# Performance work log

Hardware: AMD Instinct MI355X
Metric: run time of the kernel (lower is better)

The kernel has to match this reference:

```python
import jax, jax.numpy as jnp
import numpy as np

UNITS = 1000


def gru_step(x, h, W, U, b):
    # Keras GRU, reset_after=True. b: [2, 3*units] = (input bias, recurrent bias)
    gx = x @ W + b[0]
    gh = h @ U + b[1]
    xz, xr, xh = jnp.split(gx, 3, axis=-1)
    hz, hr, hh_ = jnp.split(gh, 3, axis=-1)
    z = jax.nn.sigmoid(xz + hz)
    r = jax.nn.sigmoid(xr + hr)
    hh = jnp.tanh(xh + r * hh_)
    return z * h + (1.0 - z) * hh


def setup_inputs() -> dict:
    key = jax.random.key(0)
    ks = jax.random.split(key, 12)
    V1, E, U = 32001, 100, UNITS
    B, S = 64, 25
    sc = 0.05
    return {
        "x": jax.random.randint(ks[0], (B, S), 0, V1, dtype=jnp.int32),
        "target": jax.random.randint(ks[1], (B, S), 0, V1, dtype=jnp.int32),
        "start_token": 2,
        "emb_table": jax.random.normal(ks[2], (V1, E), jnp.float32) * sc,
        "enc_kernel": jax.random.normal(ks[3], (E, 3 * U), jnp.float32) * sc,
        "enc_recurrent": jax.random.normal(ks[4], (U, 3 * U), jnp.float32) * sc,
        "enc_bias": jax.random.normal(ks[5], (2, 3 * U), jnp.float32) * sc,
        "dec_kernel": jax.random.normal(ks[6], (E, 3 * U), jnp.float32) * sc,
        "dec_recurrent": jax.random.normal(ks[7], (U, 3 * U), jnp.float32) * sc,
        "dec_bias": jax.random.normal(ks[8], (2, 3 * U), jnp.float32) * sc,
        "fc_w": jax.random.normal(ks[9], (U, V1), jnp.float32) * sc,
        "fc_b": jnp.zeros((V1,), jnp.float32),
    }


def reference(x, target, start_token, emb_table, enc_kernel, enc_recurrent,
              enc_bias, dec_kernel, dec_recurrent, dec_bias, fc_w, fc_b):
    B, S = x.shape
    max_len = target.shape[1]

    # ---- Encoder (computed faithfully; its output is unused downstream,
    # matching the original where attention is never invoked) ----
    emb_x = emb_table[x]                      # [B,S,E]
    mask_x = (x != 0)                          # mask_zero embedding

    def enc_scan(h, xm):
        xt, mt = xm                            # xt:[B,E], mt:[B]
        hn = gru_step(xt, h, enc_kernel, enc_recurrent, enc_bias)
        h = jnp.where(mt[:, None], hn, h)      # masked steps carry state
        return h, h

    h0 = jnp.zeros((B, UNITS), emb_x.dtype)
    enc_state, enc_out = jax.lax.scan(
        enc_scan, h0, (jnp.swapaxes(emb_x, 0, 1), jnp.swapaxes(mask_x, 0, 1)))

    # ---- Decoder: original calls gru WITHOUT initial_state, so every step
    # starts from a zero hidden state -> all timesteps are independent. ----
    # teacher-forced inputs: [start_token, target[:, :-1]]
    tokens = jnp.concatenate(
        [jnp.full((B, 1), start_token, dtype=target.dtype), target[:, :-1]], axis=1)  # [B,T]
    emb_d = emb_table[tokens]                  # [B,T,E]
    mask_d = (tokens != 0)                     # [B,T]

    h_zero = jnp.zeros((B, max_len, UNITS), emb_d.dtype)
    h1 = gru_step(emb_d, h_zero, dec_kernel, dec_recurrent, dec_bias)  # [B,T,U]
    # masked single step -> output is the zero initial output
    h1 = jnp.where(mask_d[..., None], h1, 0.0)

    logits = h1 @ fc_w + fc_b                  # [B,T,V+1]
    app_emb = logits.astype(jnp.float32) @ emb_table  # [B,T,E]
    return app_emb
```

## Files before the change

### kernel.cpp

```cpp
#include <hip/hip_runtime.h>

typedef _Float16 half_t;
typedef _Float16 half8 __attribute__((ext_vector_type(8)));
typedef float    floatx4 __attribute__((ext_vector_type(4)));

#define V1     32001
#define EMBD   100
#define UNITS  1000
#define SEQ    25
#define NROWS  1600
#define KPAD   32032
#define HSTR   1024
#define NKB    32
#define PROWS  1024

__global__ __launch_bounds__(256) void kPre(
    const float* __restrict__ E, half_t* __restrict__ ET,
    const float* __restrict__ fcb, float* __restrict__ vvec,
    const int* __restrict__ target, const int* __restrict__ stok,
    const float* __restrict__ K, const float* __restrict__ bias,
    half_t* __restrict__ h1h)
{
    __shared__ char smem[100 * 66 * sizeof(half_t)];
    const int tid = threadIdx.x;
    const int bid = blockIdx.x;

    if (bid < 501) {
        half_t* lds = (half_t*)smem;
        const int k0 = bid * 64;
        const int e  = tid & 127;
        const int kh = tid >> 7;
        for (int kk = kh; kk < 64; kk += 2) {
            const int k = k0 + kk;
            float v = 0.f;
            if (k < 32000 && e < 100) v = E[k * 100 + e];
            if (e < 100) lds[e * 66 + kk] = (half_t)v;
        }
        __syncthreads();
        const int kl = tid & 63;
        const int eh = tid >> 6;
        if (k0 + kl < KPAD) {
            for (int ee = eh; ee < 100; ee += 4)
                ET[(long)ee * KPAD + k0 + kl] = lds[ee * 66 + kl];
        }
        return;
    }

    if (bid < 757) {
        const int e  = tid & 127;
        const int g  = tid >> 7;
        const int ec = min(e, 99);
        const int slice = (bid - 501) * 2 + g;
        const int chunk = (V1 + 511) / 512;
        const int j0 = slice * chunk;
        const int j1 = min(j0 + chunk, V1);
        float acc = 0.f;
        for (int j = j0; j < j1; ++j)
            acc += fcb[j] * E[j * 100 + ec];
        if (e < 100) atomicAdd(&vvec[e], acc);
        return;
    }

    float (*xs)[100] = (float(*)[100])smem;
    __shared__ int msk[8];
    const int b3    = bid - 757;
    const int rg    = b3 % 200;
    const int uc    = b3 / 200;
    const int ibase = rg * 8;
    {
        const int r = tid >> 5, c = tid & 31;
        const int i = ibase + r;
        const int bb = i / SEQ, t = i - bb * SEQ;
        const int token = (t == 0) ? stok[0] : target[bb * SEQ + t - 1];
        if (c == 0) msk[r] = (token != 0);
        for (int cc = c; cc < 100; cc += 32)
            xs[r][cc] = E[token * 100 + cc];
    }
    __syncthreads();

    const int u = uc * 256 + tid;
    if (u < UNITS) {
        float az[8], ar[8], ah[8];
#pragma unroll
        for (int r = 0; r < 8; ++r) { az[r] = 0.f; ar[r] = 0.f; ah[r] = 0.f; }
#pragma unroll 4
        for (int k = 0; k < 100; ++k) {
            const float wz = K[k * 3000 + u];
            const float wr = K[k * 3000 + 1000 + u];
            const float wh = K[k * 3000 + 2000 + u];
#pragma unroll
            for (int r = 0; r < 8; ++r) {
                const float x = xs[r][k];
                az[r] += x * wz;
                ar[r] += x * wr;
                ah[r] += x * wh;
            }
        }
        const float* b0 = bias;
        const float* b1 = bias + 3000;
        const float bz  = b0[u] + b1[u];
        const float br  = b0[1000 + u] + b1[1000 + u];
        const float bh0 = b0[2000 + u];
        const float bh1 = b1[2000 + u];
#pragma unroll
        for (int r = 0; r < 8; ++r) {
            const float z   = 1.f / (1.f + __expf(-(az[r] + bz)));
            const float rg_ = 1.f / (1.f + __expf(-(ar[r] + br)));
            const float pre = ah[r] + bh0 + rg_ * bh1;
            const float ex  = __expf(2.f * pre);
            const float hh  = 1.f - 2.f / (ex + 1.f);
            h1h[(ibase + r) * HSTR + u] = (half_t)(msk[r] ? (1.f - z) * hh : 0.f);
        }
    } else {
        const half_t cv = (half_t)((u == 1000) ? 1.f : 0.f);
#pragma unroll
        for (int r = 0; r < 8; ++r)
            h1h[(ibase + r) * HSTR + u] = cv;
    }
}

__global__ __launch_bounds__(256) void kA(const float* __restrict__ W,
                                          const half_t* __restrict__ ET,
                                          float* __restrict__ P)
{
    __shared__ float red[3][64][57];
    const int tid   = threadIdx.x;
    const int lane  = tid & 63;
    const int wv    = tid >> 6;
    const int mb    = blockIdx.x;
    const int kb    = blockIdx.y;
    const int row16 = lane & 15;
    const int quad  = lane >> 4;

    const int m0  = mb * 32 + row16;
    const int mc0 = min(m0, UNITS - 1);
    const int mc1 = min(m0 + 16, UNITS - 1);

    const int ub = kb * 32;
    const int ue = min(ub + 32, 1000);
    const int pw = (ue - ub + 3) >> 2;
    const int wb = ub + wv * pw;
    const int we = min(wb + pw, ue);

    floatx4 acc0[7], acc1[7];
#pragma unroll
    for (int t = 0; t < 7; ++t) {
        acc0[t] = (floatx4){0.f, 0.f, 0.f, 0.f};
        acc1[t] = (floatx4){0.f, 0.f, 0.f, 0.f};
    }

    const float* wrow0 = W + (long)mc0 * V1;
    const float* wrow1 = W + (long)mc1 * V1;
    const half_t* bbase[7];
#pragma unroll
    for (int t = 0; t < 7; ++t) {
        const int nc = min(t * 16 + row16, 99);
        bbase[t] = ET + (long)nc * KPAD + quad * 8;
    }

    int un = wb;
    for (; un + 2 <= we; un += 2) {
        float f[2][16];
#pragma unroll
        for (int j = 0; j < 2; ++j) {
            const int k0 = (un + j) * 32 + quad * 8;
            __builtin_memcpy(&f[j][0], wrow0 + k0, 32);
            __builtin_memcpy(&f[j][8], wrow1 + k0, 32);
        }
#pragma unroll
        for (int j = 0; j < 2; ++j) {
            half8 a0, a1;
#pragma unroll
            for (int q = 0; q < 8; ++q) {
                a0[q] = (half_t)f[j][q];
                a1[q] = (half_t)f[j][8 + q];
            }
            const int koff = (un + j) * 32;
#pragma unroll
            for (int t = 0; t < 7; ++t) {
                const half8 b = *(const half8*)(bbase[t] + koff);
                acc0[t] = __builtin_amdgcn_mfma_f32_16x16x32_f16(a0, b, acc0[t], 0, 0, 0);
                acc1[t] = __builtin_amdgcn_mfma_f32_16x16x32_f16(a1, b, acc1[t], 0, 0, 0);
            }
        }
    }
    for (; un < we; ++un) {
        const int k0 = un * 32 + quad * 8;
        float f0[8], f1[8];
        __builtin_memcpy(f0, wrow0 + k0, 32);
        __builtin_memcpy(f1, wrow1 + k0, 32);
        half8 a0, a1;
#pragma unroll
        for (int q = 0; q < 8; ++q) { a0[q] = (half_t)f0[q]; a1[q] = (half_t)f1[q]; }
#pragma unroll
        for (int t = 0; t < 7; ++t) {
            const half8 b = *(const half8*)(bbase[t] + un * 32);
            acc0[t] = __builtin_amdgcn_mfma_f32_16x16x32_f16(a0, b, acc0[t], 0, 0, 0);
            acc1[t] = __builtin_amdgcn_mfma_f32_16x16x32_f16(a1, b, acc1[t], 0, 0, 0);
        }
    }

    if (wv > 0) {
#pragma unroll
        for (int t = 0; t < 7; ++t)
#pragma unroll
            for (int r = 0; r < 4; ++r) {
                red[wv - 1][lane][t * 4 + r]      = acc0[t][r];
                red[wv - 1][lane][28 + t * 4 + r] = acc1[t][r];
            }
    }
    __syncthreads();
    if (wv == 0) {
        float* Pk = P + (long)kb * (PROWS * 100);
        const int orow0 = mb * 32 + quad * 4;
#pragma unroll
        for (int t = 0; t < 7; ++t) {
            const int col = t * 16 + row16;
            if (col < 100) {
#pragma unroll
                for (int r = 0; r < 4; ++r) {
                    const int i = t * 4 + r;
                    const float s0 = acc0[t][r] + red[0][lane][i]
                                   + red[1][lane][i] + red[2][lane][i];
                    const float s1 = acc1[t][r] + red[0][lane][28 + i]
                                   + red[1][lane][28 + i] + red[2][lane][28 + i];
                    Pk[(orow0 + r) * 100 + col]      = s0;
                    Pk[(orow0 + 16 + r) * 100 + col] = s1;
                }
            }
        }
    }
}

__global__ __launch_bounds__(256) void kPost(const float* __restrict__ P,
                                             const float* __restrict__ W,
                                             const float* __restrict__ E,
                                             const float* __restrict__ vvec,
                                             half_t* __restrict__ MbT)
{
    const int idx = blockIdx.x * 256 + threadIdx.x;
    const int kk  = idx / 100;
    const int e   = idx - kk * 100;
    float s;
    if (kk < 1000) {
        s = 0.f;
#pragma unroll
        for (int kb = 0; kb < NKB; ++kb)
            s += P[(long)kb * (PROWS * 100) + kk * 100 + e];
        s += W[(long)kk * V1 + 32000] * E[32000 * 100 + e];
    } else if (kk == 1000) {
        s = vvec[e];
    } else {
        s = 0.f;
    }
    MbT[e * HSTR + kk] = (half_t)s;
}

__global__ __launch_bounds__(256) void kC(const half_t* __restrict__ h1h,
                                          const half_t* __restrict__ MbT,
                                          float* __restrict__ out)
{
    __shared__ float red[3][64][29];
    const int tid   = threadIdx.x;
    const int lane  = tid & 63;
    const int wv    = tid >> 6;
    const int rb    = blockIdx.x;
    const int row16 = lane & 15;
    const int quad  = lane >> 4;

    const half_t* arow = h1h + (long)(rb * 16 + row16) * HSTR + quad * 8;
    const half_t* bbase[7];
#pragma unroll
    for (int t = 0; t < 7; ++t) {
        const int nc = min(t * 16 + row16, 99);
        bbase[t] = MbT + (long)nc * HSTR + quad * 8;
    }

    floatx4 acc[7];
#pragma unroll
    for (int t = 0; t < 7; ++t) acc[t] = (floatx4){0.f, 0.f, 0.f, 0.f};

    const int wb = wv * 8;
#pragma unroll 2
    for (int un = wb; un < wb + 8; ++un) {
        const half8 a = *(const half8*)(arow + un * 32);
#pragma unroll
        for (int t = 0; t < 7; ++t) {
            const half8 b = *(const half8*)(bbase[t] + un * 32);
            acc[t] = __builtin_amdgcn_mfma_f32_16x16x32_f16(a, b, acc[t], 0, 0, 0);
        }
    }

    if (wv > 0) {
#pragma unroll
        for (int t = 0; t < 7; ++t)
#pragma unroll
            for (int r = 0; r < 4; ++r)
                red[wv - 1][lane][t * 4 + r] = acc[t][r];
    }
    __syncthreads();
    if (wv == 0) {
        const int orow0 = rb * 16 + quad * 4;
#pragma unroll
        for (int t = 0; t < 7; ++t) {
            const int col = t * 16 + row16;
            if (col < 100) {
#pragma unroll
                for (int r = 0; r < 4; ++r) {
                    const int i = t * 4 + r;
                    out[(orow0 + r) * 100 + col] = acc[t][r] + red[0][lane][i]
                        + red[1][lane][i] + red[2][lane][i];
                }
            }
        }
    }
}

extern "C" void kernel_launch(void* const* d_in, const int* in_sizes, int n_in,
                              void* d_out, int out_size, void* d_ws, size_t ws_size,
                              hipStream_t stream)
{
    const int*   target     = (const int*)d_in[1];
    const int*   start_tok  = (const int*)d_in[2];
    const float* emb        = (const float*)d_in[3];
    const float* dec_kernel = (const float*)d_in[7];
    const float* dec_bias   = (const float*)d_in[9];
    const float* fc_w       = (const float*)d_in[10];
    const float* fc_b       = (const float*)d_in[11];

    float*  vvec = (float*)d_ws;
    half_t* ET   = (half_t*)(vvec + 128);
    half_t* h1h  = ET + (size_t)100 * KPAD;
    half_t* MbT  = h1h + (size_t)NROWS * HSTR;
    float*  P    = (float*)(MbT + (size_t)100 * HSTR);
    float*  out  = (float*)d_out;

    hipMemsetAsync(vvec, 0, 128 * sizeof(float), stream);

    kPre<<<1557, 256, 0, stream>>>(emb, ET, fc_b, vvec, target, start_tok,
                                   dec_kernel, dec_bias, h1h);
    kA<<<dim3(32, NKB), 256, 0, stream>>>(fc_w, ET, P);
    kPost<<<(PROWS * 100) / 256, 256, 0, stream>>>(P, fc_w, emb, vvec, MbT);
    kC<<<100, 256, 0, stream>>>(h1h, MbT, out);
}
```

Before: 318.6 us.

## Give each kA wave its own row tile and drop the in-block LDS reduction

kA is restructured so that each wave owns a separate 16-row slice of fc_w (64 rows per block) instead of the four waves splitting K and reducing through LDS. The K split moves entirely to the grid: 36 chunks of 28 units, with the partials summed later in kPost. The inner loop now batches loads for four K-steps before issuing the MFMAs, to keep more memory requests in flight. In exchange, each B (embedding) fragment now feeds one MFMA instead of two, so embedding reads roughly double, and there are more partial slices for kPost to read and sum.

```diff
diff --git a/kernel.cpp b/kernel.cpp
--- a/kernel.cpp
+++ b/kernel.cpp
@@ -11,7 +11,8 @@
 #define NROWS  1600
 #define KPAD   32032
 #define HSTR   1024
-#define NKB    32
+#define NKB    36
+#define KUQ    28
 #define PROWS  1024
 
 __global__ __launch_bounds__(256) void kPre(
@@ -123,111 +124,81 @@
                                           const half_t* __restrict__ ET,
                                           float* __restrict__ P)
 {
-    __shared__ float red[3][64][57];
     const int tid   = threadIdx.x;
     const int lane  = tid & 63;
     const int wv    = tid >> 6;
-    const int mb    = blockIdx.x;
-    const int kb    = blockIdx.y;
+    const int mgrp  = blockIdx.x;
+    const int kq    = blockIdx.y;
     const int row16 = lane & 15;
     const int quad  = lane >> 4;
 
-    const int m0  = mb * 32 + row16;
-    const int mc0 = min(m0, UNITS - 1);
-    const int mc1 = min(m0 + 16, UNITS - 1);
-
-    const int ub = kb * 32;
-    const int ue = min(ub + 32, 1000);
-    const int pw = (ue - ub + 3) >> 2;
-    const int wb = ub + wv * pw;
-    const int we = min(wb + pw, ue);
-
-    floatx4 acc0[7], acc1[7];
-#pragma unroll
-    for (int t = 0; t < 7; ++t) {
-        acc0[t] = (floatx4){0.f, 0.f, 0.f, 0.f};
-        acc1[t] = (floatx4){0.f, 0.f, 0.f, 0.f};
-    }
-
-    const float* wrow0 = W + (long)mc0 * V1;
-    const float* wrow1 = W + (long)mc1 * V1;
-    const half_t* bbase[7];
+    const int m  = mgrp * 64 + wv * 16 + row16;
+    const int mc = min(m, UNITS - 1);
+    const float* wrow = W + (long)mc * V1;
+
+    const int wb = kq * KUQ;
+    const int we = min(wb + KUQ, 1000);
+
+    floatx4 acc[7];
+#pragma unroll
+    for (int t = 0; t < 7; ++t) acc[t] = (floatx4){0.f, 0.f, 0.f, 0.f};
+
+    const half_t* bb[7];
 #pragma unroll
     for (int t = 0; t < 7; ++t) {
         const int nc = min(t * 16 + row16, 99);
-        bbase[t] = ET + (long)nc * KPAD + quad * 8;
+        bb[t] = ET + (long)nc * KPAD + quad * 8;
     }
 
     int un = wb;
-    for (; un + 2 <= we; un += 2) {
-        float f[2][16];
-#pragma unroll
-        for (int j = 0; j < 2; ++j) {
+    for (; un + 4 <= we; un += 4) {
+        float fa[4][8];
+        half8 vb[4][7];
+#pragma unroll
+        for (int j = 0; j < 4; ++j) {
             const int k0 = (un + j) * 32 + quad * 8;
-            __builtin_memcpy(&f[j][0], wrow0 + k0, 32);
-            __builtin_memcpy(&f[j][8], wrow1 + k0, 32);
-        }
-#pragma unroll
-        for (int j = 0; j < 2; ++j) {
-            half8 a0, a1;
-#pragma unroll
-            for (int q = 0; q < 8; ++q) {
-                a0[q] = (half_t)f[j][q];
-                a1[q] = (half_t)f[j][8 + q];
-            }
+            __builtin_memcpy(&fa[j][0], wrow + k0, 32);
+        }
+#pragma unroll
+        for (int j = 0; j < 4; ++j) {
             const int koff = (un + j) * 32;
 #pragma unroll
-            for (int t = 0; t < 7; ++t) {
-                const half8 b = *(const half8*)(bbase[t] + koff);
-                acc0[t] = __builtin_amdgcn_mfma_f32_16x16x32_f16(a0, b, acc0[t], 0, 0, 0);
-                acc1[t] = __builtin_amdgcn_mfma_f32_16x16x32_f16(a1, b, acc1[t], 0, 0, 0);
-            }
+            for (int t = 0; t < 7; ++t)
+                vb[j][t] = *(const half8*)(bb[t] + koff);
+        }
+#pragma unroll
+        for (int j = 0; j < 4; ++j) {
+            half8 a;
+#pragma unroll
+            for (int q = 0; q < 8; ++q) a[q] = (half_t)fa[j][q];
+#pragma unroll
+            for (int t = 0; t < 7; ++t)
+                acc[t] = __builtin_amdgcn_mfma_f32_16x16x32_f16(a, vb[j][t], acc[t], 0, 0, 0);
         }
     }
     for (; un < we; ++un) {
         const int k0 = un * 32 + quad * 8;
-        float f0[8], f1[8];
-        __builtin_memcpy(f0, wrow0 + k0, 32);
-        __builtin_memcpy(f1, wrow1 + k0, 32);
-        half8 a0, a1;
-#pragma unroll
-        for (int q = 0; q < 8; ++q) { a0[q] = (half_t)f0[q]; a1[q] = (half_t)f1[q]; }
+        float f0[8];
+        __builtin_memcpy(f0, wrow + k0, 32);
+        half8 a;
+#pragma unroll
+        for (int q = 0; q < 8; ++q) a[q] = (half_t)f0[q];
 #pragma unroll
         for (int t = 0; t < 7; ++t) {
-            const half8 b = *(const half8*)(bbase[t] + un * 32);
-            acc0[t] = __builtin_amdgcn_mfma_f32_16x16x32_f16(a0, b, acc0[t], 0, 0, 0);
-            acc1[t] = __builtin_amdgcn_mfma_f32_16x16x32_f16(a1, b, acc1[t], 0, 0, 0);
-        }
-    }
-
-    if (wv > 0) {
-#pragma unroll
-        for (int t = 0; t < 7; ++t)
-#pragma unroll
-            for (int r = 0; r < 4; ++r) {
-                red[wv - 1][lane][t * 4 + r]      = acc0[t][r];
-                red[wv - 1][lane][28 + t * 4 + r] = acc1[t][r];
-            }
-    }
-    __syncthreads();
-    if (wv == 0) {
-        float* Pk = P + (long)kb * (PROWS * 100);
-        const int orow0 = mb * 32 + quad * 4;
-#pragma unroll
-        for (int t = 0; t < 7; ++t) {
-            const int col = t * 16 + row16;
-            if (col < 100) {
-#pragma unroll
-                for (int r = 0; r < 4; ++r) {
-                    const int i = t * 4 + r;
-                    const float s0 = acc0[t][r] + red[0][lane][i]
-                                   + red[1][lane][i] + red[2][lane][i];
-                    const float s1 = acc1[t][r] + red[0][lane][28 + i]
-                                   + red[1][lane][28 + i] + red[2][lane][28 + i];
-                    Pk[(orow0 + r) * 100 + col]      = s0;
-                    Pk[(orow0 + 16 + r) * 100 + col] = s1;
-                }
-            }
+            const half8 b = *(const half8*)(bb[t] + un * 32);
+            acc[t] = __builtin_amdgcn_mfma_f32_16x16x32_f16(a, b, acc[t], 0, 0, 0);
+        }
+    }
+
+    float* Pk = P + (long)kq * (PROWS * 100);
+    const int orow0 = mgrp * 64 + wv * 16 + quad * 4;
+#pragma unroll
+    for (int t = 0; t < 7; ++t) {
+        const int col = t * 16 + row16;
+        if (col < 100) {
+#pragma unroll
+            for (int r = 0; r < 4; ++r)
+                Pk[(orow0 + r) * 100 + col] = acc[t][r];
         }
     }
 }
@@ -244,7 +215,7 @@
     float s;
     if (kk < 1000) {
         s = 0.f;
-#pragma unroll
+#pragma unroll 4
         for (int kb = 0; kb < NKB; ++kb)
             s += P[(long)kb * (PROWS * 100) + kk * 100 + e];
         s += W[(long)kk * V1 + 32000] * E[32000 * 100 + e];
@@ -339,7 +310,7 @@
 
     kPre<<<1557, 256, 0, stream>>>(emb, ET, fc_b, vvec, target, start_tok,
                                    dec_kernel, dec_bias, h1h);
-    kA<<<dim3(32, NKB), 256, 0, stream>>>(fc_w, ET, P);
+    kA<<<dim3(16, NKB), 256, 0, stream>>>(fc_w, ET, P);
     kPost<<<(PROWS * 100) / 256, 256, 0, stream>>>(P, fc_w, emb, vvec, MbT);
     kC<<<100, 256, 0, stream>>>(h1h, MbT, out);
 }
```

Result: slower. 348.5 us (+9.4%).
